# Optimization experiments

Hardware: AMD Instinct MI355X
Metric: run time of the kernel (lower is better)

## Reference

```python
import jax, jax.numpy as jnp
import numpy as np

B, W, D = 8, 1024, 1024
HEADS, KDIM, VDIM = 16, 64, 64


def setup_inputs() -> dict:
    key = jax.random.key(0)
    k1, k2, k3, k4 = jax.random.split(key, 4)
    # he_normal-ish scaling for weights
    s = (2.0 / D) ** 0.5
    return {
        "inputs": jax.random.normal(k1, (B, W, D), dtype=jnp.float32),
        "Wq": jax.random.normal(k2, (D, HEADS * KDIM), dtype=jnp.float32) * s,
        "Wk": jax.random.normal(k3, (D, HEADS * KDIM), dtype=jnp.float32) * s,
        "Wv": jax.random.normal(k4, (D, HEADS * VDIM), dtype=jnp.float32) * s,
    }


def reference(inputs, Wq, Wk, Wv):
    # Self-attention: memory = inputs
    bsz, win, _ = inputs.shape
    # DenseHeads: linear projection, reshaped to (B, W, heads, head_units)
    q = (inputs @ Wq).reshape(bsz, win, HEADS, KDIM)
    k = (inputs @ Wk).reshape(bsz, win, HEADS, KDIM)
    v = (inputs @ Wv).reshape(bsz, win, HEADS, VDIM)
    scale = KDIM ** (-0.5)
    # scores[b,q,h,m] = sum_k Q[b,q,h,k] * K[b,m,h,k]
    scores = jnp.einsum("bqhk,bmhk->bqhm", q, k) * scale
    attn = jax.nn.softmax(scores, axis=-1)
    # out[b,q,h,v] = sum_m attn[b,q,h,m] * V[b,m,h,v]
    out = jnp.einsum("bqhm,bmhv->bqhv", attn, v)
    return out
```

## Files before the change

kernel.cpp:

```cpp
#include <hip/hip_runtime.h>
#include <stdint.h>


using bf16x8 = __attribute__((ext_vector_type(8))) __bf16;
using f32x4  = __attribute__((ext_vector_type(4))) float;
using f16x4  = __attribute__((ext_vector_type(4))) _Float16;

union frag_u  { uint4 u4; bf16x8 f; };
union vfrag_u { uint2 u2; f16x4 f; };
union pfrag_u { unsigned int u[2]; f16x4 f; };

__device__ inline unsigned short f2bf(float x){
  unsigned int u = __float_as_uint(x);
  u += 0x7fffu + ((u >> 16) & 1u);
  return (unsigned short)(u >> 16);
}

__device__ inline unsigned int pkrtz_u32(float a, float b){
  auto r = __builtin_amdgcn_cvt_pkrtz(a, b);
  unsigned int u; __builtin_memcpy(&u, &r, 4); return u;
}

__device__ inline void gl_lds16(const void* g, void* l){
  __builtin_amdgcn_global_load_lds(
      (const __attribute__((address_space(1))) void*)g,
      (__attribute__((address_space(3))) void*)l, 16, 0, 0);
}

#define SBAR() do{ asm volatile("" ::: "memory"); __builtin_amdgcn_s_barrier(); asm volatile("" ::: "memory"); }while(0)
#define LGKM0() asm volatile("s_waitcnt lgkmcnt(0)" ::: "memory")
#define VMC(n)  asm volatile("s_waitcnt vmcnt(" #n ")" ::: "memory")

__global__ void cast_all(const float* __restrict__ X,
                         const float* __restrict__ Wq, const float* __restrict__ Wk,
                         const float* __restrict__ Wv,
                         unsigned short* __restrict__ Xb,
                         unsigned short* __restrict__ Wt){
  __shared__ float tile[64][65];
  int bid = blockIdx.x;
  if (bid < 8192){
    int i = (bid * 256 + threadIdx.x) * 4;
    float4 v = *(const float4*)(X + i);
    ushort4 o;
    o.x = f2bf(v.x); o.y = f2bf(v.y); o.z = f2bf(v.z); o.w = f2bf(v.w);
    *(ushort4*)(Xb + i) = o;
    return;
  }
  int id = bid - 8192;
  int proj = id >> 8;
  int rem  = id & 255;
  int kt = rem & 15, nt = rem >> 4;
  const float* Wsrc = (proj == 0) ? Wq : ((proj == 1) ? Wk : Wv);
  int k0 = kt * 64, n0 = nt * 64;
  int tx = threadIdx.x & 63, ty = threadIdx.x >> 6;
  for (int i = 0; i < 16; i++){
    int k = i * 4 + ty;
    tile[k][tx] = Wsrc[(k0 + k) * 1024 + n0 + tx];
  }
  __syncthreads();
  for (int i = 0; i < 16; i++){
    int n = i * 4 + ty;
    Wt[(proj * 1024 + n0 + n) * 1024 + k0 + tx] = f2bf(tile[tx][n]);
  }
}


__device__ __forceinline__ void tile_step(
    const unsigned short* __restrict__ Xb,
    const unsigned short* __restrict__ Wt,
    const char* Ab, const char* Bb, char* AbN, char* BbS,
    const int* aoff, const int* boff, int t, int w,
    int aRdS, int bRdS, f32x4 acc[8][3])
{
  frag_u bfr[3][2];
#pragma unroll
  for (int n = 0; n < 3; n++)
#pragma unroll
    for (int kk = 0; kk < 2; kk++)
      bfr[n][kk].u4 = *(const uint4*)(Bb + bRdS + n * 2048 + kk * 64);

#pragma unroll
  for (int p = 0; p < 4; p++){
    frag_u afr[2][2];
#pragma unroll
    for (int i = 0; i < 2; i++)
#pragma unroll
      for (int kk = 0; kk < 2; kk++)
        afr[i][kk].u4 = *(const uint4*)(Ab + aRdS + (p * 2 + i) * 2048 + kk * 64);
    if (p == 0){
      gl_lds16(Xb + aoff[0] + (t + 1) * 64, AbN + (0 * 8 + w) * 1024);
      gl_lds16(Xb + aoff[1] + (t + 1) * 64, AbN + (1 * 8 + w) * 1024);
    } else if (p == 1){
      gl_lds16(Xb + aoff[2] + (t + 1) * 64, AbN + (2 * 8 + w) * 1024);
      gl_lds16(Xb + aoff[3] + (t + 1) * 64, AbN + (3 * 8 + w) * 1024);
    } else if (p == 2){
      gl_lds16(Wt + boff[0] + (t + 2) * 64, BbS + (0 * 8 + w) * 1024);
      gl_lds16(Wt + boff[1] + (t + 2) * 64, BbS + (1 * 8 + w) * 1024);
    } else {
      gl_lds16(Wt + boff[2] + (t + 2) * 64, BbS + (2 * 8 + w) * 1024);
    }
    SBAR();
    LGKM0();
    __builtin_amdgcn_s_setprio(1);
#pragma unroll
    for (int kk = 0; kk < 2; kk++)
#pragma unroll
      for (int i = 0; i < 2; i++)
#pragma unroll
        for (int n = 0; n < 3; n++)
          acc[p * 2 + i][n] = __builtin_amdgcn_mfma_f32_16x16x32_bf16(
              afr[i][kk].f, bfr[n][kk].f, acc[p * 2 + i][n], 0, 0, 0);
    __builtin_amdgcn_s_setprio(0);
    if (p == 3) VMC(3);
    SBAR();
  }
}

__global__ __launch_bounds__(512, 2) void gemm_qkv(
    const unsigned short* __restrict__ Xb,
    const unsigned short* __restrict__ Wt,
    unsigned short* __restrict__ QK,
    unsigned short* __restrict__ Vt){
  __shared__ __align__(16) char Abuf[2][32768];
  __shared__ __align__(16) char Bbuf[2][24576];

  int bid = blockIdx.x;
  int tau = (bid & 7) * 64 + (bid >> 3);
  int by = tau >> 4, bx = tau & 15;
  int tid = threadIdx.x;
  int w = tid >> 6, lane = tid & 63;
  int li = lane & 15, g = lane >> 4;
  int wr = w >> 2, wc = w & 3;

  int aoff[4], boff[3];
#pragma unroll
  for (int j = 0; j < 4; j++){
    int s = ((j * 8 + w) << 10) + (lane << 4);
    int p = s ^ (((s >> 9) & 1) << 5);
    aoff[j] = (by * 256 + (p >> 7)) * 1024 + ((p & 127) >> 1);
  }
#pragma unroll
  for (int j = 0; j < 3; j++){
    int s = ((j * 8 + w) << 10) + (lane << 4);
    int p = s ^ (((s >> 9) & 1) << 5);
    boff[j] = (bx * 192 + (p >> 7)) * 1024 + ((p & 127) >> 1);
  }
  int swzbit = ((li >> 2) & 1) << 5;
  int aRdS = ((wr * 128 + li) * 128 + g * 16) ^ swzbit;
  int bRdS = ((wc * 48  + li) * 128 + g * 16) ^ swzbit;

  f32x4 acc[8][3] = {};

  gl_lds16(Wt + boff[0], Bbuf[0] + (0 * 8 + w) * 1024);
  gl_lds16(Wt + boff[1], Bbuf[0] + (1 * 8 + w) * 1024);
  gl_lds16(Wt + boff[2], Bbuf[0] + (2 * 8 + w) * 1024);
#pragma unroll
  for (int j = 0; j < 4; j++)
    gl_lds16(Xb + aoff[j], Abuf[0] + (j * 8 + w) * 1024);
  gl_lds16(Wt + boff[0] + 64, Bbuf[1] + (0 * 8 + w) * 1024);
  gl_lds16(Wt + boff[1] + 64, Bbuf[1] + (1 * 8 + w) * 1024);
  gl_lds16(Wt + boff[2] + 64, Bbuf[1] + (2 * 8 + w) * 1024);
  VMC(3);
  SBAR();

  for (int t = 0; t < 16; t += 2){
    tile_step(Xb, Wt, Abuf[0], Bbuf[0], Abuf[1], Bbuf[0], aoff, boff, t,     w, aRdS, bRdS, acc);
    tile_step(Xb, Wt, Abuf[1], Bbuf[1], Abuf[0], Bbuf[1], aoff, boff, t + 1, w, aRdS, bRdS, acc);
  }

  int row0 = by * 256 + wr * 128 + g * 4;
  int bb16 = (by >> 2) * 16;
#pragma unroll
  for (int n = 0; n < 3; n++){
    int cb = bx * 192 + wc * 48 + n * 16;
    if (cb < 2048){
      float sc = (cb < 1024) ? 0.1803368801111f : 1.0f;
#pragma unroll
      for (int m = 0; m < 8; m++){
        int row = row0 + m * 16;
#pragma unroll
        for (int r = 0; r < 4; r++)
          QK[(size_t)(row + r) * 2048 + cb + li] = f2bf(acc[m][n][r] * sc);
      }
    } else {
      int vc = cb + li - 2048;
      int hh = vc >> 6, dd = vc & 63;
#pragma unroll
      for (int m = 0; m < 8; m++){
        int mtok = (row0 + m * 16) & 1023;
        uint2 cv;
        cv.x = pkrtz_u32(acc[m][n][0], acc[m][n][1]);
        cv.y = pkrtz_u32(acc[m][n][2], acc[m][n][3]);
        *(uint2*)(Vt + ((size_t)(bb16 + hh) * 64 + dd) * 1024 + mtok) = cv;
      }
    }
  }
  VMC(0);
}

__global__ __launch_bounds__(256, 4) void attn(const unsigned short* __restrict__ QK,
                                               const unsigned short* __restrict__ Vt,
                                               float* __restrict__ Out){
  __shared__ __align__(16) unsigned short Kbuf[64 * 64];
  __shared__ __align__(16) unsigned short Vbuf[64 * 64];
  int id = blockIdx.x;
  int bh = id & 127, qb = id >> 7;
  int b = bh >> 4, h = bh & 15;
  int w = threadIdx.x >> 6, lane = threadIdx.x & 63;
  int g = lane >> 4, li = lane & 15;
  int lrow = lane >> 3, lcol = lane & 7;
  int scol = ((lcol ^ lrow) & 7) * 8;

  frag_u qf[2];
  {
    int tok = b * 1024 + qb * 64 + w * 16 + li;
    const unsigned short* qp = QK + (size_t)tok * 2048 + h * 64 + g * 8;
    qf[0].u4 = *(const uint4*)(qp);
    qf[1].u4 = *(const uint4*)(qp + 32);
  }

  f32x4 o[4] = {};
  f32x4 osum = {};
  const f32x4 bias = {-10.f, -10.f, -10.f, -10.f};
  pfrag_u ones;
  ones.u[0] = 0x3c003c00u; ones.u[1] = 0x3c003c00u;

  const unsigned short* Kg = QK + (size_t)b * 1024 * 2048 + 1024 + h * 64;
  const unsigned short* Vg = Vt + (size_t)bh * 65536;

  for (int mt = 0; mt < 16; mt++){
    int m0 = mt * 64;
    __syncthreads();
    for (int i = 0; i < 2; i++){
      int idx = w * 2 + i;
      int row = idx * 8 + lrow;
      gl_lds16(Kg + (size_t)(m0 + row) * 2048 + scol, Kbuf + idx * 512);
      gl_lds16(Vg + row * 1024 + m0 + scol,           Vbuf + idx * 512);
    }
    __syncthreads();

    f32x4 s[4];
    for (int t = 0; t < 4; t++) s[t] = bias;
    for (int t = 0; t < 4; t++){
      for (int c = 0; c < 2; c++){
        frag_u kf;
        kf.u4 = *(const uint4*)(Kbuf + (t * 16 + li) * 64 + ((((c << 2) + g) ^ (li & 7)) << 3));
        s[t] = __builtin_amdgcn_mfma_f32_16x16x32_bf16(kf.f, qf[c].f, s[t], 0, 0, 0);
      }
    }

    pfrag_u pf[4];
    for (int t = 0; t < 4; t++){
      float p0 = __builtin_exp2f(s[t][0]);
      float p1 = __builtin_exp2f(s[t][1]);
      float p2 = __builtin_exp2f(s[t][2]);
      float p3 = __builtin_exp2f(s[t][3]);
      pf[t].u[0] = pkrtz_u32(p0, p1);
      pf[t].u[1] = pkrtz_u32(p2, p3);
    }

    for (int t = 0; t < 4; t++)
      osum = __builtin_amdgcn_mfma_f32_16x16x16f16(ones.f, pf[t].f, osum, 0, 0, 0);
    for (int tv = 0; tv < 4; tv++){
      for (int t = 0; t < 4; t++){
        int gg = ((t * 2 + (g >> 1)) ^ (li & 7));
        vfrag_u vf;
        vf.u2 = *(const uint2*)(Vbuf + (tv * 16 + li) * 64 + gg * 8 + (g & 1) * 4);
        o[tv] = __builtin_amdgcn_mfma_f32_16x16x16f16(vf.f, pf[t].f, o[tv], 0, 0, 0);
      }
    }
  }

  float inv = 1.f / osum[0];

  int tok = b * 1024 + qb * 64 + w * 16 + li;
  float* op = Out + (size_t)tok * 1024 + h * 64 + g * 4;
  for (int tv = 0; tv < 4; tv++){
    float4 v4;
    v4.x = o[tv][0] * inv; v4.y = o[tv][1] * inv;
    v4.z = o[tv][2] * inv; v4.w = o[tv][3] * inv;
    *(float4*)(op + tv * 16) = v4;
  }
}

extern "C" void kernel_launch(void* const* d_in, const int* in_sizes, int n_in,
                              void* d_out, int out_size, void* d_ws, size_t ws_size,
                              hipStream_t stream) {
  const float* X  = (const float*)d_in[0];
  const float* Wq = (const float*)d_in[1];
  const float* Wk = (const float*)d_in[2];
  const float* Wv = (const float*)d_in[3];
  float* Out = (float*)d_out;
  char* ws = (char*)d_ws;
  unsigned short* Xb = (unsigned short*)(ws);
  unsigned short* Wt = (unsigned short*)(ws + (size_t)16 * 1024 * 1024);
  unsigned short* QK = (unsigned short*)(ws + (size_t)22 * 1024 * 1024);
  unsigned short* Vt = (unsigned short*)(ws + (size_t)54 * 1024 * 1024);

  cast_all<<<8960, 256, 0, stream>>>(X, Wq, Wk, Wv, Xb, Wt);
  gemm_qkv<<<512, 512, 0, stream>>>(Xb, Wt, QK, Vt);
  attn    <<<2048, 256, 0, stream>>>(QK, Vt, Out);
}
```

Measured before the change: 213.0 us.

## Restructure QKV GEMM main loop with double-buffered A fragments and XOR swizzle

```diff
diff --git a/kernel.cpp b/kernel.cpp
--- a/kernel.cpp
+++ b/kernel.cpp
@@ -28,7 +28,6 @@
 }
 
 #define SBAR() do{ asm volatile("" ::: "memory"); __builtin_amdgcn_s_barrier(); asm volatile("" ::: "memory"); }while(0)
-#define LGKM0() asm volatile("s_waitcnt lgkmcnt(0)" ::: "memory")
 #define VMC(n)  asm volatile("s_waitcnt vmcnt(" #n ")" ::: "memory")
 
 __global__ void cast_all(const float* __restrict__ X,
@@ -64,58 +63,6 @@
   }
 }
 
-
-__device__ __forceinline__ void tile_step(
-    const unsigned short* __restrict__ Xb,
-    const unsigned short* __restrict__ Wt,
-    const char* Ab, const char* Bb, char* AbN, char* BbS,
-    const int* aoff, const int* boff, int t, int w,
-    int aRdS, int bRdS, f32x4 acc[8][3])
-{
-  frag_u bfr[3][2];
-#pragma unroll
-  for (int n = 0; n < 3; n++)
-#pragma unroll
-    for (int kk = 0; kk < 2; kk++)
-      bfr[n][kk].u4 = *(const uint4*)(Bb + bRdS + n * 2048 + kk * 64);
-
-#pragma unroll
-  for (int p = 0; p < 4; p++){
-    frag_u afr[2][2];
-#pragma unroll
-    for (int i = 0; i < 2; i++)
-#pragma unroll
-      for (int kk = 0; kk < 2; kk++)
-        afr[i][kk].u4 = *(const uint4*)(Ab + aRdS + (p * 2 + i) * 2048 + kk * 64);
-    if (p == 0){
-      gl_lds16(Xb + aoff[0] + (t + 1) * 64, AbN + (0 * 8 + w) * 1024);
-      gl_lds16(Xb + aoff[1] + (t + 1) * 64, AbN + (1 * 8 + w) * 1024);
-    } else if (p == 1){
-      gl_lds16(Xb + aoff[2] + (t + 1) * 64, AbN + (2 * 8 + w) * 1024);
-      gl_lds16(Xb + aoff[3] + (t + 1) * 64, AbN + (3 * 8 + w) * 1024);
-    } else if (p == 2){
-      gl_lds16(Wt + boff[0] + (t + 2) * 64, BbS + (0 * 8 + w) * 1024);
-      gl_lds16(Wt + boff[1] + (t + 2) * 64, BbS + (1 * 8 + w) * 1024);
-    } else {
-      gl_lds16(Wt + boff[2] + (t + 2) * 64, BbS + (2 * 8 + w) * 1024);
-    }
-    SBAR();
-    LGKM0();
-    __builtin_amdgcn_s_setprio(1);
-#pragma unroll
-    for (int kk = 0; kk < 2; kk++)
-#pragma unroll
-      for (int i = 0; i < 2; i++)
-#pragma unroll
-        for (int n = 0; n < 3; n++)
-          acc[p * 2 + i][n] = __builtin_amdgcn_mfma_f32_16x16x32_bf16(
-              afr[i][kk].f, bfr[n][kk].f, acc[p * 2 + i][n], 0, 0, 0);
-    __builtin_amdgcn_s_setprio(0);
-    if (p == 3) VMC(3);
-    SBAR();
-  }
-}
-
 __global__ __launch_bounds__(512, 2) void gemm_qkv(
     const unsigned short* __restrict__ Xb,
     const unsigned short* __restrict__ Wt,
@@ -130,43 +77,82 @@
   int tid = threadIdx.x;
   int w = tid >> 6, lane = tid & 63;
   int li = lane & 15, g = lane >> 4;
+  int lrow = lane >> 3;
   int wr = w >> 2, wc = w & 3;
 
+  int xcol = ((lane & 7) ^ lrow) << 3;
   int aoff[4], boff[3];
 #pragma unroll
-  for (int j = 0; j < 4; j++){
-    int s = ((j * 8 + w) << 10) + (lane << 4);
-    int p = s ^ (((s >> 9) & 1) << 5);
-    aoff[j] = (by * 256 + (p >> 7)) * 1024 + ((p & 127) >> 1);
-  }
-#pragma unroll
-  for (int j = 0; j < 3; j++){
-    int s = ((j * 8 + w) << 10) + (lane << 4);
-    int p = s ^ (((s >> 9) & 1) << 5);
-    boff[j] = (bx * 192 + (p >> 7)) * 1024 + ((p & 127) >> 1);
-  }
-  int swzbit = ((li >> 2) & 1) << 5;
-  int aRdS = ((wr * 128 + li) * 128 + g * 16) ^ swzbit;
-  int bRdS = ((wc * 48  + li) * 128 + g * 16) ^ swzbit;
+  for (int j = 0; j < 4; j++)
+    aoff[j] = (by * 256 + (j * 8 + w) * 8 + lrow) * 1024 + xcol;
+#pragma unroll
+  for (int j = 0; j < 3; j++)
+    boff[j] = (bx * 192 + (j * 8 + w) * 8 + lrow) * 1024 + xcol;
+
+  int swz  = (li & 7) << 4;
+  int colA0 = (g * 16) ^ swz;
+  int colA1 = (64 + g * 16) ^ swz;
+  int aBase = (wr * 128 + li) * 128;
+  int bBase = (wc * 48 + li) * 128;
 
   f32x4 acc[8][3] = {};
-
-  gl_lds16(Wt + boff[0], Bbuf[0] + (0 * 8 + w) * 1024);
-  gl_lds16(Wt + boff[1], Bbuf[0] + (1 * 8 + w) * 1024);
-  gl_lds16(Wt + boff[2], Bbuf[0] + (2 * 8 + w) * 1024);
-#pragma unroll
-  for (int j = 0; j < 4; j++)
-    gl_lds16(Xb + aoff[j], Abuf[0] + (j * 8 + w) * 1024);
-  gl_lds16(Wt + boff[0] + 64, Bbuf[1] + (0 * 8 + w) * 1024);
-  gl_lds16(Wt + boff[1] + 64, Bbuf[1] + (1 * 8 + w) * 1024);
-  gl_lds16(Wt + boff[2] + 64, Bbuf[1] + (2 * 8 + w) * 1024);
+  frag_u bfr[3][2], a0[2][2], a1[2][2];
+
+#define STA(buf, j, tt) gl_lds16(Xb + aoff[j] + (tt) * 64, &Abuf[buf][((j) * 8 + w) * 1024])
+#define STB(buf, j, tt) gl_lds16(Wt + boff[j] + (tt) * 64, &Bbuf[buf][((j) * 8 + w) * 1024])
+#define LDA(S, buf, m0) do{ \
+  S[0][0].u4 = *(const uint4*)&Abuf[buf][aBase + (m0)     * 2048 + colA0]; \
+  S[0][1].u4 = *(const uint4*)&Abuf[buf][aBase + (m0)     * 2048 + colA1]; \
+  S[1][0].u4 = *(const uint4*)&Abuf[buf][aBase + (m0 + 1) * 2048 + colA0]; \
+  S[1][1].u4 = *(const uint4*)&Abuf[buf][aBase + (m0 + 1) * 2048 + colA1]; }while(0)
+#define LDB(buf) do{ \
+  _Pragma("unroll") for (int n = 0; n < 3; n++){ \
+    bfr[n][0].u4 = *(const uint4*)&Bbuf[buf][bBase + n * 2048 + colA0]; \
+    bfr[n][1].u4 = *(const uint4*)&Bbuf[buf][bBase + n * 2048 + colA1]; } }while(0)
+#define MFMAP(S, P) do{ __builtin_amdgcn_s_setprio(1); \
+  _Pragma("unroll") for (int kk = 0; kk < 2; kk++) \
+  _Pragma("unroll") for (int i = 0; i < 2; i++) \
+  _Pragma("unroll") for (int n = 0; n < 3; n++) \
+    acc[(P) * 2 + i][n] = __builtin_amdgcn_mfma_f32_16x16x32_bf16( \
+        S[i][kk].f, bfr[n][kk].f, acc[(P) * 2 + i][n], 0, 0, 0); \
+  __builtin_amdgcn_s_setprio(0); }while(0)
+
+  STB(0, 0, 0); STB(0, 1, 0); STB(0, 2, 0);
+  STA(0, 0, 0); STA(0, 1, 0); STA(0, 2, 0); STA(0, 3, 0);
+  STB(1, 0, 1); STB(1, 1, 1); STB(1, 2, 1);
   VMC(3);
   SBAR();
 
-  for (int t = 0; t < 16; t += 2){
-    tile_step(Xb, Wt, Abuf[0], Bbuf[0], Abuf[1], Bbuf[0], aoff, boff, t,     w, aRdS, bRdS, acc);
-    tile_step(Xb, Wt, Abuf[1], Bbuf[1], Abuf[0], Bbuf[1], aoff, boff, t + 1, w, aRdS, bRdS, acc);
-  }
+  for (int t = 0; t < 16; ++t){
+    int cur = t & 1, nxt = cur ^ 1;
+    LDB(cur); LDA(a0, cur, 0);
+    LDA(a1, cur, 2);
+    if (t < 15){ STA(nxt, 0, t + 1); STA(nxt, 1, t + 1); }
+    SBAR();
+    MFMAP(a0, 0);
+    SBAR();
+    LDA(a0, cur, 4);
+    if (t < 15){ STA(nxt, 2, t + 1); STA(nxt, 3, t + 1); }
+    SBAR();
+    MFMAP(a1, 1);
+    SBAR();
+    LDA(a1, cur, 6);
+    if (t < 14){ STB(cur, 0, t + 2); STB(cur, 1, t + 2); }
+    SBAR();
+    MFMAP(a0, 2);
+    SBAR();
+    if (t < 14) STB(cur, 2, t + 2);
+    SBAR();
+    MFMAP(a1, 3);
+    if (t < 14) { VMC(3); }
+    else if (t == 14) { VMC(0); }
+    SBAR();
+  }
+#undef STA
+#undef STB
+#undef LDA
+#undef LDB
+#undef MFMAP
 
   int row0 = by * 256 + wr * 128 + g * 4;
   int bb16 = (by >> 2) * 16;
@@ -195,7 +181,6 @@
       }
     }
   }
-  VMC(0);
 }
 
 __global__ __launch_bounds__(256, 4) void attn(const unsigned short* __restrict__ QK,
```

Result: no change. 214.1 us (+0.5%).
